# Performance work log

Measured on AMD Instinct MI355X. Metric: run time of the kernel, lower is better.

Reference implementation:

```python
import jax, jax.numpy as jnp
import numpy as np

GROUP_SIZE = 64
OUT_F, IN_F = 11008, 4096
W_SHAPE = (OUT_F, IN_F)


def quantize_q40(w):
    # w: fp32 weight, numel divisible by GROUP_SIZE
    wg = w.reshape(-1, GROUP_SIZE)                      # [N, G]
    wmax = jnp.max(jnp.abs(wg), axis=1)
    scale = (wmax / 7.0).astype(jnp.float16)[:, None]   # [N, 1] fp16 per-group scale
    quant = wg / scale.astype(jnp.float32)
    q = jnp.round(quant).astype(jnp.int8)               # values in [-7, 7]
    pairs = q.reshape(-1, 2, GROUP_SIZE)                # even rows -> MSB nibble, odd -> LSB
    packed = ((pairs[:, 0] << 4) | (pairs[:, 1] & 15)).astype(jnp.int8)  # [N/2, G]
    return packed, scale


def dequantize_q40(w, scale):
    # w: int8 packed [N/2, G]; arithmetic shifts sign-extend each nibble
    msb = w >> 4
    lsb = (w << 4) >> 4
    full = jnp.concatenate([msb, lsb], axis=1).reshape(-1, GROUP_SIZE)  # interleave back to [N, G]
    return (full.astype(jnp.float16) * scale).reshape(W_SHAPE)


def setup_inputs() -> dict:
    key = jax.random.key(0)
    kx, kw = jax.random.split(key)
    x = jax.random.normal(kx, (4, 2048, IN_F), dtype=jnp.float16)
    w_fp = jax.random.normal(kw, W_SHAPE, dtype=jnp.float32) * 0.02
    linear_w, linear_s = quantize_q40(w_fp)
    return {"x": x, "linear_w": linear_w, "linear_s": linear_s}


def reference(x, linear_w, linear_s):
    # dequantize packed int4 weights to fp16, then dense linear (no bias)
    deq = dequantize_q40(linear_w, linear_s)            # [OUT_F, IN_F] fp16
    return jnp.einsum('bsi,oi->bso', x, deq)            # F.linear(x, deq)
```

## Files before the change

### kernel.cpp

```cpp
#include <hip/hip_runtime.h>
#include <stdint.h>

#define IN_F   4096
#define OUT_F  11008
#define M_ROWS 8192
#define BM 256
#define BN 256
#define BK 64
#define NTILE_K (IN_F / BK)

typedef __attribute__((ext_vector_type(4))) float  f32x4;
typedef __attribute__((ext_vector_type(4))) int    int4v;
typedef __attribute__((ext_vector_type(8))) unsigned short ushort8;
typedef __bf16 bf16x8 __attribute__((ext_vector_type(8)));

__device__ __forceinline__ unsigned short f2bf(float f) {
  unsigned int u = __builtin_bit_cast(unsigned int, f);
  u += 0x7fffu + ((u >> 16) & 1u);
  return (unsigned short)(u >> 16);
}

__global__ __launch_bounds__(256) void dequant_q40(const int* __restrict__ w,
                                                   const float* __restrict__ sc,
                                                   unsigned short* __restrict__ wb) {
  const int total8 = (OUT_F * IN_F) / 8;
  for (int t = blockIdx.x * blockDim.x + threadIdx.x; t < total8;
       t += gridDim.x * blockDim.x) {
    const int f0  = t * 8;
    const int p   = f0 >> 7;
    const int nib = (f0 >> 6) & 1;
    const int j0  = f0 & 63;
    const float scale = sc[f0 >> 6];
    const int* src = w + p * 64 + j0;
    const int4v b0 = __builtin_nontemporal_load(reinterpret_cast<const int4v*>(src));
    const int4v b1 = __builtin_nontemporal_load(reinterpret_cast<const int4v*>(src + 4));
    ushort8 r;
#pragma unroll
    for (int e = 0; e < 4; ++e) {
      const int v0 = b0[e], v1 = b1[e];
      const int q0 = nib ? ((v0 << 28) >> 28) : (v0 >> 4);
      const int q1 = nib ? ((v1 << 28) >> 28) : (v1 >> 4);
      r[e]     = f2bf((float)q0 * scale);
      r[4 + e] = f2bf((float)q1 * scale);
    }
    *reinterpret_cast<ushort8*>(wb + f0) = r;
  }
}

__global__ __launch_bounds__(256) void cvt_x(const float* __restrict__ x,
                                             unsigned short* __restrict__ xb) {
  const int total8 = (M_ROWS * IN_F) / 8;
  for (int t = blockIdx.x * blockDim.x + threadIdx.x; t < total8;
       t += gridDim.x * blockDim.x) {
    const f32x4 a0 = __builtin_nontemporal_load(reinterpret_cast<const f32x4*>(x + t * 8));
    const f32x4 a1 = __builtin_nontemporal_load(reinterpret_cast<const f32x4*>(x + t * 8 + 4));
    ushort8 r;
#pragma unroll
    for (int e = 0; e < 4; ++e) {
      r[e]     = f2bf(a0[e]);
      r[4 + e] = f2bf(a1[e]);
    }
    *reinterpret_cast<ushort8*>(xb + t * 8) = r;
  }
}

__device__ __forceinline__ void gld16(const void* g, void* l) {
  __builtin_amdgcn_global_load_lds(
      (const __attribute__((address_space(1))) unsigned int*)(uintptr_t)g,
      (__attribute__((address_space(3))) unsigned int*)(unsigned int)(uintptr_t)l,
      16, 0, 0);
}

#define BAR() do { asm volatile("" ::: "memory"); __builtin_amdgcn_s_barrier(); \
                   asm volatile("" ::: "memory"); } while (0)

__global__ __launch_bounds__(512, 2) void gemm_bt(const unsigned short* __restrict__ A,
                                                  const unsigned short* __restrict__ B,
                                                  float* __restrict__ C) {
  __shared__ __align__(16) unsigned short lds[65536];

  const int NT  = OUT_F / BN;
  const int nwg = (M_ROWS / BM) * NT;
  const int cpx = nwg >> 3;
  const int bid = blockIdx.x;
  const int swz = (bid & 7) * cpx + (bid >> 3);
  const int mt  = swz / NT;
  const int nt  = swz - mt * NT;

  const int tid  = threadIdx.x;
  const int lane = tid & 63;
  const int wid  = tid >> 6;
  const int wr   = wid >> 2;
  const int wc   = wid & 3;

  const int r_st = tid >> 2;
  const int lc   = (tid & 3) ^ ((tid >> 3) & 3);
  const unsigned short* gA = A + (size_t)(mt * BM + r_st) * IN_F + lc * 8;
  const unsigned short* gB = B + (size_t)(nt * BM + r_st) * IN_F + lc * 8;
  unsigned short* ldsw = lds + tid * 8;

#define STAGE_A(b, h, kk) do {                                              \
    unsigned short* d_ = ldsw + (b) * 32768 + (h) * 8192;                   \
    const unsigned short* s_ = gA + (kk) + (h) * 32;                        \
    gld16(s_, d_); gld16(s_ + (size_t)128 * IN_F, d_ + 4096);               \
  } while (0)
#define STAGE_B(b, h, kk) do {                                              \
    unsigned short* d_ = ldsw + (b) * 32768 + 16384 + (h) * 8192;           \
    const unsigned short* s_ = gB + (kk) + (h) * 32;                        \
    gld16(s_, d_); gld16(s_ + (size_t)128 * IN_F, d_ + 4096);               \
  } while (0)

  const int fr   = lane & 15;
  const int kq   = lane >> 4;
  const int coff = (kq ^ ((fr >> 1) & 3)) * 8;

  bf16x8 afr[4], bfr[4];
#define RD_A(b, h, mq) do {                                                 \
    const unsigned short* p_ = lds + (b) * 32768 + (h) * 8192 + coff;       \
    _Pragma("unroll") for (int mm = 0; mm < 4; ++mm)                        \
      afr[mm] = *reinterpret_cast<const bf16x8*>(                           \
          p_ + (size_t)(wr * 128 + (mq) * 64 + mm * 16 + fr) * 32);         \
  } while (0)
#define RD_B(b, h) do {                                                     \
    const unsigned short* p_ = lds + (b) * 32768 + 16384 + (h) * 8192 + coff; \
    _Pragma("unroll") for (int nn = 0; nn < 4; ++nn)                        \
      bfr[nn] = *reinterpret_cast<const bf16x8*>(                           \
          p_ + (size_t)(wc * 64 + nn * 16 + fr) * 32);                      \
  } while (0)

  f32x4 acc[8][4] = {};
#define MFMA16(mq) do {                                                     \
    __builtin_amdgcn_s_setprio(1);                                          \
    _Pragma("unroll") for (int mm = 0; mm < 4; ++mm)                        \
      _Pragma("unroll") for (int nn = 0; nn < 4; ++nn)                      \
        acc[(mq)*4+mm][nn] = __builtin_amdgcn_mfma_f32_16x16x32_bf16(       \
            afr[mm], bfr[nn], acc[(mq)*4+mm][nn], 0, 0, 0);                 \
    __builtin_amdgcn_s_setprio(0);                                          \
  } while (0)

#define VWAIT8() asm volatile("s_waitcnt vmcnt(8)" ::: "memory")

  STAGE_A(0, 0, 0); STAGE_B(0, 0, 0);
  STAGE_A(0, 1, 0); STAGE_B(0, 1, 0);
  STAGE_A(1, 0, BK); STAGE_B(1, 0, BK);
  VWAIT8();
  BAR();

  for (int it = 0; it < NTILE_K / 2; ++it) {
    const int kt1 = ((2 * it + 1) & (NTILE_K - 1)) * BK;
    const int kt2 = ((2 * it + 2) & (NTILE_K - 1)) * BK;
    const int kt3 = ((2 * it + 3) & (NTILE_K - 1)) * BK;

    RD_A(0, 0, 0); RD_B(0, 0); STAGE_A(1, 1, kt1);
    BAR(); MFMA16(0);
    RD_A(0, 0, 1); STAGE_B(1, 1, kt1); VWAIT8();
    BAR(); MFMA16(1);
    RD_A(0, 1, 0); RD_B(0, 1); STAGE_A(0, 0, kt2);
    BAR(); MFMA16(0);
    RD_A(0, 1, 1); STAGE_B(0, 0, kt2); VWAIT8();
    BAR(); MFMA16(1);
    RD_A(1, 0, 0); RD_B(1, 0); STAGE_A(0, 1, kt2);
    BAR(); MFMA16(0);
    RD_A(1, 0, 1); STAGE_B(0, 1, kt2); VWAIT8();
    BAR(); MFMA16(1);
    RD_A(1, 1, 0); RD_B(1, 1); STAGE_A(1, 0, kt3);
    BAR(); MFMA16(0);
    RD_A(1, 1, 1); STAGE_B(1, 0, kt3); VWAIT8();
    BAR(); MFMA16(1);
  }

  const int col  = nt * BN + wc * 64 + fr;
  const int row0 = mt * BM + wr * 128 + (lane >> 4) * 4;
#pragma unroll
  for (int m = 0; m < 8; ++m) {
#pragma unroll
    for (int n = 0; n < 4; ++n) {
      float* cp = C + (size_t)(row0 + m * 16) * OUT_F + (col + n * 16);
#pragma unroll
      for (int r = 0; r < 4; ++r) cp[(size_t)r * OUT_F] = acc[m][n][r];
    }
  }
}

extern "C" void kernel_launch(void* const* d_in, const int* in_sizes, int n_in,
                              void* d_out, int out_size, void* d_ws, size_t ws_size,
                              hipStream_t stream) {
  const float* x = (const float*)d_in[0];
  const int*   w = (const int*)d_in[1];
  const float* s = (const float*)d_in[2];
  float*     out = (float*)d_out;

  unsigned short* wb = (unsigned short*)d_ws;
  unsigned short* xb = wb + (size_t)OUT_F * IN_F;

  dequant_q40<<<dim3(2048), dim3(256), 0, stream>>>(w, s, wb);
  cvt_x<<<dim3(2048), dim3(256), 0, stream>>>(x, xb);
  gemm_bt<<<dim3((M_ROWS / BM) * (OUT_F / BN)), dim3(512), 0, stream>>>(xb, wb, out);
}
```

Before: 743.8 us.

## Double-buffer MFMA operand registers to prefetch LDS fragments one step ahead

Splits the A and B fragment registers into two alternating sets, so LDS reads for the next MFMA block are issued before the current block's MFMAs run. The stage schedule is reordered and the vmcnt wait is tightened to 6 to match. This is meant to hide LDS read latency behind matrix math. In exchange it raises VGPR pressure under the 512-thread, 2-block launch bound and relies on careful barrier and buffer ordering to avoid reading stale LDS data.

```diff
diff --git a/kernel.cpp b/kernel.cpp
--- a/kernel.cpp
+++ b/kernel.cpp
@@ -114,59 +114,60 @@
   const int kq   = lane >> 4;
   const int coff = (kq ^ ((fr >> 1) & 3)) * 8;
 
-  bf16x8 afr[4], bfr[4];
-#define RD_A(b, h, mq) do {                                                 \
+  bf16x8 aS0[4], aS1[4], bS0[4], bS1[4];
+#define RD_A(dst, b, h, mq) do {                                            \
     const unsigned short* p_ = lds + (b) * 32768 + (h) * 8192 + coff;       \
     _Pragma("unroll") for (int mm = 0; mm < 4; ++mm)                        \
-      afr[mm] = *reinterpret_cast<const bf16x8*>(                           \
+      dst[mm] = *reinterpret_cast<const bf16x8*>(                           \
           p_ + (size_t)(wr * 128 + (mq) * 64 + mm * 16 + fr) * 32);         \
   } while (0)
-#define RD_B(b, h) do {                                                     \
+#define RD_B(dst, b, h) do {                                                \
     const unsigned short* p_ = lds + (b) * 32768 + 16384 + (h) * 8192 + coff; \
     _Pragma("unroll") for (int nn = 0; nn < 4; ++nn)                        \
-      bfr[nn] = *reinterpret_cast<const bf16x8*>(                           \
+      dst[nn] = *reinterpret_cast<const bf16x8*>(                           \
           p_ + (size_t)(wc * 64 + nn * 16 + fr) * 32);                      \
   } while (0)
 
   f32x4 acc[8][4] = {};
-#define MFMA16(mq) do {                                                     \
+#define MFMA16(mq, aset, bset) do {                                         \
     __builtin_amdgcn_s_setprio(1);                                          \
     _Pragma("unroll") for (int mm = 0; mm < 4; ++mm)                        \
       _Pragma("unroll") for (int nn = 0; nn < 4; ++nn)                      \
         acc[(mq)*4+mm][nn] = __builtin_amdgcn_mfma_f32_16x16x32_bf16(       \
-            afr[mm], bfr[nn], acc[(mq)*4+mm][nn], 0, 0, 0);                 \
+            aset[mm], bset[nn], acc[(mq)*4+mm][nn], 0, 0, 0);               \
     __builtin_amdgcn_s_setprio(0);                                          \
   } while (0)
 
-#define VWAIT8() asm volatile("s_waitcnt vmcnt(8)" ::: "memory")
+#define VWAIT6() asm volatile("s_waitcnt vmcnt(6)" ::: "memory")
 
   STAGE_A(0, 0, 0); STAGE_B(0, 0, 0);
   STAGE_A(0, 1, 0); STAGE_B(0, 1, 0);
   STAGE_A(1, 0, BK); STAGE_B(1, 0, BK);
-  VWAIT8();
+  asm volatile("s_waitcnt vmcnt(8)" ::: "memory");
   BAR();
+  RD_A(aS0, 0, 0, 0); RD_B(bS0, 0, 0);
 
   for (int it = 0; it < NTILE_K / 2; ++it) {
     const int kt1 = ((2 * it + 1) & (NTILE_K - 1)) * BK;
     const int kt2 = ((2 * it + 2) & (NTILE_K - 1)) * BK;
     const int kt3 = ((2 * it + 3) & (NTILE_K - 1)) * BK;
 
-    RD_A(0, 0, 0); RD_B(0, 0); STAGE_A(1, 1, kt1);
-    BAR(); MFMA16(0);
-    RD_A(0, 0, 1); STAGE_B(1, 1, kt1); VWAIT8();
-    BAR(); MFMA16(1);
-    RD_A(0, 1, 0); RD_B(0, 1); STAGE_A(0, 0, kt2);
-    BAR(); MFMA16(0);
-    RD_A(0, 1, 1); STAGE_B(0, 0, kt2); VWAIT8();
-    BAR(); MFMA16(1);
-    RD_A(1, 0, 0); RD_B(1, 0); STAGE_A(0, 1, kt2);
-    BAR(); MFMA16(0);
-    RD_A(1, 0, 1); STAGE_B(0, 1, kt2); VWAIT8();
-    BAR(); MFMA16(1);
-    RD_A(1, 1, 0); RD_B(1, 1); STAGE_A(1, 0, kt3);
-    BAR(); MFMA16(0);
-    RD_A(1, 1, 1); STAGE_B(1, 0, kt3); VWAIT8();
-    BAR(); MFMA16(1);
+    STAGE_A(1, 1, kt1); RD_A(aS1, 0, 0, 1); VWAIT6();
+    BAR(); MFMA16(0, aS0, bS0);
+    STAGE_B(1, 1, kt1); RD_A(aS0, 0, 1, 0); RD_B(bS1, 0, 1);
+    BAR(); MFMA16(1, aS1, bS0);
+    STAGE_A(0, 0, kt2); RD_A(aS1, 0, 1, 1); VWAIT6();
+    BAR(); MFMA16(0, aS0, bS1);
+    STAGE_B(0, 0, kt2); RD_A(aS0, 1, 0, 0); RD_B(bS0, 1, 0);
+    BAR(); MFMA16(1, aS1, bS1);
+    STAGE_A(0, 1, kt2); RD_A(aS1, 1, 0, 1); VWAIT6();
+    BAR(); MFMA16(0, aS0, bS0);
+    STAGE_B(0, 1, kt2); RD_A(aS0, 1, 1, 0); RD_B(bS1, 1, 1);
+    BAR(); MFMA16(1, aS1, bS0);
+    STAGE_A(1, 0, kt3); RD_A(aS1, 1, 1, 1); VWAIT6();
+    BAR(); MFMA16(0, aS0, bS1);
+    STAGE_B(1, 0, kt3); RD_A(aS0, 0, 0, 0); RD_B(bS0, 0, 0);
+    BAR(); MFMA16(1, aS1, bS1);
   }
 
   const int col  = nt * BN + wc * 64 + fr;
```

Measured after the change: 745.3 us. About the same (+0.2%).
